# Kernel optimization log

Measured on AMD Instinct MI355X. Metric: run time of the kernel, lower is better.

Reference implementation:

```python
import jax, jax.numpy as jnp
import numpy as np

H = 20  # hidden size (hard-coded in the module)

def setup_inputs() -> dict:
    key = jax.random.key(0)
    ks = jax.random.split(key, 7)
    B, T = 4096, 1000
    s = 1.0 / np.sqrt(H)  # torch default init bound for RNN/Linear
    x = jax.random.normal(ks[0], (B, T, 1), dtype=jnp.float32)
    W_ih = jax.random.uniform(ks[1], (H, 1), jnp.float32, -s, s)
    W_hh = jax.random.uniform(ks[2], (H, H), jnp.float32, -s, s)
    b_ih = jax.random.uniform(ks[3], (H,), jnp.float32, -s, s)
    b_hh = jax.random.uniform(ks[4], (H,), jnp.float32, -s, s)
    fc_w = jax.random.uniform(ks[5], (1, H), jnp.float32, -s, s)
    fc_b = jax.random.uniform(ks[6], (1,), jnp.float32, -s, s)
    return {"x": x, "W_ih": W_ih, "W_hh": W_hh, "b_ih": b_ih,
            "b_hh": b_hh, "fc_w": fc_w, "fc_b": fc_b}

def reference(x, W_ih, W_hh, b_ih, b_hh, fc_w, fc_b):
    # x: [B, T, 1] -> time-major [T, B, 1] for scan
    B = x.shape[0]
    xt = jnp.swapaxes(x, 0, 1)
    # precompute input projection for all timesteps: [T, B, H]
    xproj = jnp.einsum('tbi,hi->tbh', xt, W_ih) + b_ih + b_hh
    h0 = jnp.zeros((B, H), dtype=x.dtype)
    def step(h, xp_t):
        h_new = jax.nn.relu(xp_t + h @ W_hh.T)
        return h_new, None
    h_last, _ = jax.lax.scan(step, h0, xproj)
    # only the last hidden state feeds the head: fc1(rnn_out[:, -1, :])
    out = h_last @ fc_w.T + fc_b  # [B, 1]
    return out
```

## Files before the change

kernel.cpp:

```cpp
#include <hip/hip_runtime.h>


#define TT 1000

typedef float v2f __attribute__((ext_vector_type(2)));

struct Col { v2f p01, p23; float v4; };

#define PIN(v)  asm volatile("" : "+v"(v))
__device__ __forceinline__ void pinc(Col& c) {
    PIN(c.p01); PIN(c.p23); PIN(c.v4);
}
__device__ __forceinline__ void keepc(const Col& c) {
    asm volatile("" :: "v"(c.p01), "v"(c.p23), "v"(c.v4));
}

template <int CTRL>
__device__ __forceinline__ float dpp_f(float v) {
    return __int_as_float(__builtin_amdgcn_update_dpp(
        0, __float_as_int(v), CTRL, 0xF, 0xF, true));
}

#define QP_XOR1 0xB1
#define QP_XOR2 0x4E
#define ROR4   0x124
#define ROR8   0x128

template <int HALF, int C1, int C2>
__device__ __forceinline__ void step(v2f xp, v2f& h01, v2f& h23, float& h4,
                                     const Col& wc0, const Col& wc1,
                                     const Col& wc2, const Col& wc3,
                                     const Col& wc4,
                                     const Col& wih, const Col& bias) {
    const v2f xs = (HALF == 0) ? xp.xx : xp.yy;
    const float xt = (HALF == 0) ? xp.x : xp.y;

    v2f  A01 = __builtin_elementwise_fma(xs, wih.p01, bias.p01);
    v2f  A23 = __builtin_elementwise_fma(xs, wih.p23, bias.p23);
    float a4 = __builtin_fmaf(xt, wih.v4, bias.v4);

#define KCOL(hs, hk, wc)                                           \
    A01 = __builtin_elementwise_fma(hs, (wc).p01, A01);            \
    A23 = __builtin_elementwise_fma(hs, (wc).p23, A23);            \
    a4  = __builtin_fmaf(hk, (wc).v4, a4);
    KCOL(h01.xx, h01.x, wc0)
    KCOL(h01.yy, h01.y, wc1)
    KCOL(h23.xx, h23.x, wc2)
    KCOL(h23.yy, h23.y, wc3)
    { const v2f h4s = {h4, h4};
      KCOL(h4s, h4, wc4) }
#undef KCOL

    float b0 = A01.x, b1 = A01.y, b2 = A23.x, b3 = A23.y, b4 = a4;
    {
        float t0 = dpp_f<C1>(b0), t1 = dpp_f<C1>(b1), t2 = dpp_f<C1>(b2),
              t3 = dpp_f<C1>(b3), t4 = dpp_f<C1>(b4);
        b0 += t0; b1 += t1; b2 += t2; b3 += t3; b4 += t4;
    }
    {
        float t0 = dpp_f<C2>(b0), t1 = dpp_f<C2>(b1), t2 = dpp_f<C2>(b2),
              t3 = dpp_f<C2>(b3), t4 = dpp_f<C2>(b4);
        b0 += t0; b1 += t1; b2 += t2; b3 += t3; b4 += t4;
    }

    const v2f z = {0.f, 0.f};
    v2f r01 = {b0, b1};
    v2f r23 = {b2, b3};
    h01 = __builtin_elementwise_max(r01, z);
    h23 = __builtin_elementwise_max(r23, z);
    h4  = fmaxf(b4, 0.f);
}

__global__ void
__attribute__((amdgpu_flat_work_group_size(64, 64), amdgpu_waves_per_eu(1, 1)))
rnn_os_kernel(const float* __restrict__ x,
              const float* __restrict__ W_ih,
              const float* __restrict__ W_hh,
              const float* __restrict__ b_ih,
              const float* __restrict__ b_hh,
              const float* __restrict__ fc_w,
              const float* __restrict__ fc_b,
              float* __restrict__ out) {
    const int tid = blockIdx.x * 64 + threadIdx.x;
    const int b   = tid >> 4;
    const int gl  = tid & 15;
    const int a   = gl >> 2;
    const int bq  = gl & 3;

    Col we0, we1, we2, we3, we4;
    Col wo0, wo1, wo2, wo3, wo4;
#define LOADC(wk, k, rbase, cbase)                                            \
    { (wk).p01 = (v2f){ W_hh[((rbase) + 0) * 20 + (cbase) + (k)],             \
                        W_hh[((rbase) + 1) * 20 + (cbase) + (k)] };           \
      (wk).p23 = (v2f){ W_hh[((rbase) + 2) * 20 + (cbase) + (k)],             \
                        W_hh[((rbase) + 3) * 20 + (cbase) + (k)] };           \
      (wk).v4  =        W_hh[((rbase) + 4) * 20 + (cbase) + (k)]; }
    LOADC(we0, 0, a * 5, bq * 5) LOADC(we1, 1, a * 5, bq * 5)
    LOADC(we2, 2, a * 5, bq * 5) LOADC(we3, 3, a * 5, bq * 5)
    LOADC(we4, 4, a * 5, bq * 5)
    LOADC(wo0, 0, bq * 5, a * 5) LOADC(wo1, 1, bq * 5, a * 5)
    LOADC(wo2, 2, bq * 5, a * 5) LOADC(wo3, 3, bq * 5, a * 5)
    LOADC(wo4, 4, bq * 5, a * 5)
#undef LOADC

    const bool eact = (bq == 0);
    const bool oact = (a == 0);
    Col wie, bie, wio, bio;
#define LOADIB(wv, bv, base, act)                                             \
    { const float* pw = W_ih + (base);                                        \
      const float* p1 = b_ih + (base);                                        \
      const float* p2 = b_hh + (base);                                        \
      (wv).p01 = (v2f){ (act) ? pw[0] : 0.f, (act) ? pw[1] : 0.f };           \
      (wv).p23 = (v2f){ (act) ? pw[2] : 0.f, (act) ? pw[3] : 0.f };           \
      (wv).v4  =        (act) ? pw[4] : 0.f;                                  \
      (bv).p01 = (v2f){ (act) ? (p1[0] + p2[0]) : 0.f,                        \
                        (act) ? (p1[1] + p2[1]) : 0.f };                      \
      (bv).p23 = (v2f){ (act) ? (p1[2] + p2[2]) : 0.f,                        \
                        (act) ? (p1[3] + p2[3]) : 0.f };                      \
      (bv).v4  =        (act) ? (p1[4] + p2[4]) : 0.f; }
    LOADIB(wie, bie, a * 5,  eact)
    LOADIB(wio, bio, bq * 5, oact)
#undef LOADIB

    pinc(we0); pinc(we1); pinc(we2); pinc(we3); pinc(we4);
    pinc(wo0); pinc(wo1); pinc(wo2); pinc(wo3); pinc(wo4);
    pinc(wie); pinc(bie); pinc(wio); pinc(bio);

    v2f h01 = {0.f, 0.f}, h23 = {0.f, 0.f};
    float h4 = 0.f;

    const float* __restrict__ xb = x + (size_t)b * TT;

#define LOAD10(P, off)                                  \
    P##0 = *(const float4*)(xb + (off));                \
    P##1 = *(const float4*)(xb + (off) + 4);            \
    P##2 = *(const float4*)(xb + (off) + 8);            \
    P##3 = *(const float4*)(xb + (off) + 12);           \
    P##4 = *(const float4*)(xb + (off) + 16);           \
    P##5 = *(const float4*)(xb + (off) + 20);           \
    P##6 = *(const float4*)(xb + (off) + 24);           \
    P##7 = *(const float4*)(xb + (off) + 28);           \
    P##8 = *(const float4*)(xb + (off) + 32);           \
    P##9 = *(const float4*)(xb + (off) + 36);

#define STEP_E(xp, H) step<H, QP_XOR1, QP_XOR2>(xp, h01, h23, h4, we0, we1, we2, we3, we4, wie, bie);
#define STEP_O(xp, H) step<H, ROR4,    ROR8   >(xp, h01, h23, h4, wo0, wo1, wo2, wo3, wo4, wio, bio);
#define RUN4(Q) {                                       \
        const v2f qlo = {Q.x, Q.y};                     \
        const v2f qhi = {Q.z, Q.w};                     \
        STEP_E(qlo, 0) STEP_O(qlo, 1)                   \
        STEP_E(qhi, 0) STEP_O(qhi, 1) }
#define RUN40(P) RUN4(P##0) RUN4(P##1) RUN4(P##2) RUN4(P##3) RUN4(P##4) \
                 RUN4(P##5) RUN4(P##6) RUN4(P##7) RUN4(P##8) RUN4(P##9)

    float4 A0, A1, A2, A3, A4, A5, A6, A7, A8, A9;
    float4 B0, B1, B2, B3, B4, B5, B6, B7, B8, B9;
    LOAD10(A, 0)
    LOAD10(B, 40)

    for (int it = 0; it < 12; ++it) {
        const int base = it * 80;
        const int nb = (it < 11) ? base + 120 : 960;

        RUN40(A)
        LOAD10(A, base + 80)
        RUN40(B)
        LOAD10(B, nb)
    }
    RUN40(A)

#undef RUN40
#undef RUN4
#undef STEP_E
#undef STEP_O
#undef LOAD10

    keepc(we0); keepc(we1); keepc(we2); keepc(we3); keepc(we4);
    keepc(wo0); keepc(wo1); keepc(wo2); keepc(wo3); keepc(wo4);
    keepc(wie); keepc(bie); keepc(wio); keepc(bio);

    float dot;
    {
        const float* pf = fc_w + bq * 5;
        float f0 = oact ? pf[0] : 0.f, f1 = oact ? pf[1] : 0.f;
        float f2 = oact ? pf[2] : 0.f, f3 = oact ? pf[3] : 0.f;
        float f4 = oact ? pf[4] : 0.f;
        dot = h01.x * f0;
        dot = __builtin_fmaf(h01.y, f1, dot);
        dot = __builtin_fmaf(h23.x, f2, dot);
        dot = __builtin_fmaf(h23.y, f3, dot);
        dot = __builtin_fmaf(h4,    f4, dot);
    }
    dot += __shfl_xor(dot, 1, 16);
    dot += __shfl_xor(dot, 2, 16);
    dot += __shfl_xor(dot, 4, 16);
    dot += __shfl_xor(dot, 8, 16);

    if (gl == 0)
        out[b] = dot + fc_b[0];
}

extern "C" void kernel_launch(void* const* d_in, const int* in_sizes, int n_in,
                              void* d_out, int out_size, void* d_ws, size_t ws_size,
                              hipStream_t stream) {
    const float* x    = (const float*)d_in[0];
    const float* W_ih = (const float*)d_in[1];
    const float* W_hh = (const float*)d_in[2];
    const float* b_ih = (const float*)d_in[3];
    const float* b_hh = (const float*)d_in[4];
    const float* fc_w = (const float*)d_in[5];
    const float* fc_b = (const float*)d_in[6];
    float* out = (float*)d_out;

    const int block = 64;
    const int grid  = (4096 * 16) / block;
    rnn_os_kernel<<<grid, block, 0, stream>>>(x, W_ih, W_hh, b_ih, b_hh,
                                              fc_w, fc_b, out);
}
```

Measured before the change: 146.7 us.

## Pack two batch rows per 16-lane group using packed v2f lanes

Each 16-lane group now processes two batch elements at once, with the v2f packed-FMA lanes holding the two batch rows instead of two hidden units. This halves the grid and makes every FMA a full packed operation, but doubles the DPP reductions per lane. The x prefetch shrinks from 20 float4 registers ahead to 4 small float4 loads per two iterations. The aims are better packed-math use and fewer waves, at the cost of more latency exposure on the x loads and fewer waves to hide the serial recurrence.

```diff
diff --git a/kernel.cpp b/kernel.cpp
--- a/kernel.cpp
+++ b/kernel.cpp
@@ -5,14 +5,29 @@
 
 typedef float v2f __attribute__((ext_vector_type(2)));
 
-struct Col { v2f p01, p23; float v4; };
+struct WRole {
+    v2f w01[5], w23[5];
+    v2f w4a, w4b, w4c;
+    v2f wih01, wih23, wih4;
+    v2f b01, b23, b4;
+};
 
 #define PIN(v)  asm volatile("" : "+v"(v))
-__device__ __forceinline__ void pinc(Col& c) {
-    PIN(c.p01); PIN(c.p23); PIN(c.v4);
-}
-__device__ __forceinline__ void keepc(const Col& c) {
-    asm volatile("" :: "v"(c.p01), "v"(c.p23), "v"(c.v4));
+__device__ __forceinline__ void pinw(WRole& W) {
+    PIN(W.w01[0]); PIN(W.w01[1]); PIN(W.w01[2]); PIN(W.w01[3]); PIN(W.w01[4]);
+    PIN(W.w23[0]); PIN(W.w23[1]); PIN(W.w23[2]); PIN(W.w23[3]); PIN(W.w23[4]);
+    PIN(W.w4a); PIN(W.w4b); PIN(W.w4c);
+    PIN(W.wih01); PIN(W.wih23); PIN(W.wih4);
+    PIN(W.b01); PIN(W.b23); PIN(W.b4);
+}
+__device__ __forceinline__ void keepw(const WRole& W) {
+    asm volatile("" :: "v"(W.w01[0]), "v"(W.w01[1]), "v"(W.w01[2]),
+                       "v"(W.w01[3]), "v"(W.w01[4]));
+    asm volatile("" :: "v"(W.w23[0]), "v"(W.w23[1]), "v"(W.w23[2]),
+                       "v"(W.w23[3]), "v"(W.w23[4]));
+    asm volatile("" :: "v"(W.w4a), "v"(W.w4b), "v"(W.w4c));
+    asm volatile("" :: "v"(W.wih01), "v"(W.wih23), "v"(W.wih4),
+                       "v"(W.b01), "v"(W.b23), "v"(W.b4));
 }
 
 template <int CTRL>
@@ -26,49 +41,55 @@
 #define ROR4   0x124
 #define ROR8   0x128
 
-template <int HALF, int C1, int C2>
-__device__ __forceinline__ void step(v2f xp, v2f& h01, v2f& h23, float& h4,
-                                     const Col& wc0, const Col& wc1,
-                                     const Col& wc2, const Col& wc3,
-                                     const Col& wc4,
-                                     const Col& wih, const Col& bias) {
-    const v2f xs = (HALF == 0) ? xp.xx : xp.yy;
-    const float xt = (HALF == 0) ? xp.x : xp.y;
-
-    v2f  A01 = __builtin_elementwise_fma(xs, wih.p01, bias.p01);
-    v2f  A23 = __builtin_elementwise_fma(xs, wih.p23, bias.p23);
-    float a4 = __builtin_fmaf(xt, wih.v4, bias.v4);
-
-#define KCOL(hs, hk, wc)                                           \
-    A01 = __builtin_elementwise_fma(hs, (wc).p01, A01);            \
-    A23 = __builtin_elementwise_fma(hs, (wc).p23, A23);            \
-    a4  = __builtin_fmaf(hk, (wc).v4, a4);
-    KCOL(h01.xx, h01.x, wc0)
-    KCOL(h01.yy, h01.y, wc1)
-    KCOL(h23.xx, h23.x, wc2)
-    KCOL(h23.yy, h23.y, wc3)
-    { const v2f h4s = {h4, h4};
-      KCOL(h4s, h4, wc4) }
-#undef KCOL
-
-    float b0 = A01.x, b1 = A01.y, b2 = A23.x, b3 = A23.y, b4 = a4;
+template <int C1, int C2>
+__device__ __forceinline__ void step(v2f xp, v2f& h0, v2f& h1, v2f& h2,
+                                     v2f& h3, v2f& h4, const WRole& W) {
+    v2f a0 = __builtin_elementwise_fma(xp, W.wih01.xx, W.b01.xx);
+    v2f a1 = __builtin_elementwise_fma(xp, W.wih01.yy, W.b01.yy);
+    v2f a2 = __builtin_elementwise_fma(xp, W.wih23.xx, W.b23.xx);
+    v2f a3 = __builtin_elementwise_fma(xp, W.wih23.yy, W.b23.yy);
+    v2f a4 = __builtin_elementwise_fma(xp, W.wih4.xx,  W.b4.xx);
+
+#define MK(HS, W0, W1, W2, W3, W4)                         \
+    a0 = __builtin_elementwise_fma(HS, W0, a0);            \
+    a1 = __builtin_elementwise_fma(HS, W1, a1);            \
+    a2 = __builtin_elementwise_fma(HS, W2, a2);            \
+    a3 = __builtin_elementwise_fma(HS, W3, a3);            \
+    a4 = __builtin_elementwise_fma(HS, W4, a4);
+    MK(h0, W.w01[0].xx, W.w01[1].xx, W.w01[2].xx, W.w01[3].xx, W.w01[4].xx)
+    MK(h1, W.w01[0].yy, W.w01[1].yy, W.w01[2].yy, W.w01[3].yy, W.w01[4].yy)
+    MK(h2, W.w23[0].xx, W.w23[1].xx, W.w23[2].xx, W.w23[3].xx, W.w23[4].xx)
+    MK(h3, W.w23[0].yy, W.w23[1].yy, W.w23[2].yy, W.w23[3].yy, W.w23[4].yy)
+    MK(h4, W.w4a.xx,    W.w4a.yy,    W.w4b.xx,    W.w4b.yy,    W.w4c.xx)
+#undef MK
+
+    float u0 = a0.x, p0 = a0.y, u1 = a1.x, p1 = a1.y, u2 = a2.x, p2 = a2.y,
+          u3 = a3.x, p3 = a3.y, u4 = a4.x, p4 = a4.y;
     {
-        float t0 = dpp_f<C1>(b0), t1 = dpp_f<C1>(b1), t2 = dpp_f<C1>(b2),
-              t3 = dpp_f<C1>(b3), t4 = dpp_f<C1>(b4);
-        b0 += t0; b1 += t1; b2 += t2; b3 += t3; b4 += t4;
+        float t0 = dpp_f<C1>(u0), s0 = dpp_f<C1>(p0),
+              t1 = dpp_f<C1>(u1), s1 = dpp_f<C1>(p1),
+              t2 = dpp_f<C1>(u2), s2 = dpp_f<C1>(p2),
+              t3 = dpp_f<C1>(u3), s3 = dpp_f<C1>(p3),
+              t4 = dpp_f<C1>(u4), s4 = dpp_f<C1>(p4);
+        u0 += t0; p0 += s0; u1 += t1; p1 += s1; u2 += t2; p2 += s2;
+        u3 += t3; p3 += s3; u4 += t4; p4 += s4;
     }
     {
-        float t0 = dpp_f<C2>(b0), t1 = dpp_f<C2>(b1), t2 = dpp_f<C2>(b2),
-              t3 = dpp_f<C2>(b3), t4 = dpp_f<C2>(b4);
-        b0 += t0; b1 += t1; b2 += t2; b3 += t3; b4 += t4;
+        float t0 = dpp_f<C2>(u0), s0 = dpp_f<C2>(p0),
+              t1 = dpp_f<C2>(u1), s1 = dpp_f<C2>(p1),
+              t2 = dpp_f<C2>(u2), s2 = dpp_f<C2>(p2),
+              t3 = dpp_f<C2>(u3), s3 = dpp_f<C2>(p3),
+              t4 = dpp_f<C2>(u4), s4 = dpp_f<C2>(p4);
+        u0 += t0; p0 += s0; u1 += t1; p1 += s1; u2 += t2; p2 += s2;
+        u3 += t3; p3 += s3; u4 += t4; p4 += s4;
     }
 
     const v2f z = {0.f, 0.f};
-    v2f r01 = {b0, b1};
-    v2f r23 = {b2, b3};
-    h01 = __builtin_elementwise_max(r01, z);
-    h23 = __builtin_elementwise_max(r23, z);
-    h4  = fmaxf(b4, 0.f);
+    h0 = __builtin_elementwise_max((v2f){u0, p0}, z);
+    h1 = __builtin_elementwise_max((v2f){u1, p1}, z);
+    h2 = __builtin_elementwise_max((v2f){u2, p2}, z);
+    h3 = __builtin_elementwise_max((v2f){u3, p3}, z);
+    h4 = __builtin_elementwise_max((v2f){u4, p4}, z);
 }
 
 __global__ void
@@ -82,122 +103,110 @@
               const float* __restrict__ fc_b,
               float* __restrict__ out) {
     const int tid = blockIdx.x * 64 + threadIdx.x;
-    const int b   = tid >> 4;
+    const int pg  = tid >> 4;
     const int gl  = tid & 15;
     const int a   = gl >> 2;
     const int bq  = gl & 3;
 
-    Col we0, we1, we2, we3, we4;
-    Col wo0, wo1, wo2, wo3, wo4;
-#define LOADC(wk, k, rbase, cbase)                                            \
-    { (wk).p01 = (v2f){ W_hh[((rbase) + 0) * 20 + (cbase) + (k)],             \
-                        W_hh[((rbase) + 1) * 20 + (cbase) + (k)] };           \
-      (wk).p23 = (v2f){ W_hh[((rbase) + 2) * 20 + (cbase) + (k)],             \
-                        W_hh[((rbase) + 3) * 20 + (cbase) + (k)] };           \
-      (wk).v4  =        W_hh[((rbase) + 4) * 20 + (cbase) + (k)]; }
-    LOADC(we0, 0, a * 5, bq * 5) LOADC(we1, 1, a * 5, bq * 5)
-    LOADC(we2, 2, a * 5, bq * 5) LOADC(we3, 3, a * 5, bq * 5)
-    LOADC(we4, 4, a * 5, bq * 5)
-    LOADC(wo0, 0, bq * 5, a * 5) LOADC(wo1, 1, bq * 5, a * 5)
-    LOADC(wo2, 2, bq * 5, a * 5) LOADC(wo3, 3, bq * 5, a * 5)
-    LOADC(wo4, 4, bq * 5, a * 5)
-#undef LOADC
-
     const bool eact = (bq == 0);
     const bool oact = (a == 0);
-    Col wie, bie, wio, bio;
-#define LOADIB(wv, bv, base, act)                                             \
-    { const float* pw = W_ih + (base);                                        \
-      const float* p1 = b_ih + (base);                                        \
-      const float* p2 = b_hh + (base);                                        \
-      (wv).p01 = (v2f){ (act) ? pw[0] : 0.f, (act) ? pw[1] : 0.f };           \
-      (wv).p23 = (v2f){ (act) ? pw[2] : 0.f, (act) ? pw[3] : 0.f };           \
-      (wv).v4  =        (act) ? pw[4] : 0.f;                                  \
-      (bv).p01 = (v2f){ (act) ? (p1[0] + p2[0]) : 0.f,                        \
-                        (act) ? (p1[1] + p2[1]) : 0.f };                      \
-      (bv).p23 = (v2f){ (act) ? (p1[2] + p2[2]) : 0.f,                        \
-                        (act) ? (p1[3] + p2[3]) : 0.f };                      \
-      (bv).v4  =        (act) ? (p1[4] + p2[4]) : 0.f; }
-    LOADIB(wie, bie, a * 5,  eact)
-    LOADIB(wio, bio, bq * 5, oact)
-#undef LOADIB
-
-    pinc(we0); pinc(we1); pinc(we2); pinc(we3); pinc(we4);
-    pinc(wo0); pinc(wo1); pinc(wo2); pinc(wo3); pinc(wo4);
-    pinc(wie); pinc(bie); pinc(wio); pinc(bio);
-
-    v2f h01 = {0.f, 0.f}, h23 = {0.f, 0.f};
-    float h4 = 0.f;
-
-    const float* __restrict__ xb = x + (size_t)b * TT;
-
-#define LOAD10(P, off)                                  \
-    P##0 = *(const float4*)(xb + (off));                \
-    P##1 = *(const float4*)(xb + (off) + 4);            \
-    P##2 = *(const float4*)(xb + (off) + 8);            \
-    P##3 = *(const float4*)(xb + (off) + 12);           \
-    P##4 = *(const float4*)(xb + (off) + 16);           \
-    P##5 = *(const float4*)(xb + (off) + 20);           \
-    P##6 = *(const float4*)(xb + (off) + 24);           \
-    P##7 = *(const float4*)(xb + (off) + 28);           \
-    P##8 = *(const float4*)(xb + (off) + 32);           \
-    P##9 = *(const float4*)(xb + (off) + 36);
-
-#define STEP_E(xp, H) step<H, QP_XOR1, QP_XOR2>(xp, h01, h23, h4, we0, we1, we2, we3, we4, wie, bie);
-#define STEP_O(xp, H) step<H, ROR4,    ROR8   >(xp, h01, h23, h4, wo0, wo1, wo2, wo3, wo4, wio, bio);
-#define RUN4(Q) {                                       \
-        const v2f qlo = {Q.x, Q.y};                     \
-        const v2f qhi = {Q.z, Q.w};                     \
-        STEP_E(qlo, 0) STEP_O(qlo, 1)                   \
-        STEP_E(qhi, 0) STEP_O(qhi, 1) }
-#define RUN40(P) RUN4(P##0) RUN4(P##1) RUN4(P##2) RUN4(P##3) RUN4(P##4) \
-                 RUN4(P##5) RUN4(P##6) RUN4(P##7) RUN4(P##8) RUN4(P##9)
-
-    float4 A0, A1, A2, A3, A4, A5, A6, A7, A8, A9;
-    float4 B0, B1, B2, B3, B4, B5, B6, B7, B8, B9;
-    LOAD10(A, 0)
-    LOAD10(B, 40)
-
-    for (int it = 0; it < 12; ++it) {
-        const int base = it * 80;
-        const int nb = (it < 11) ? base + 120 : 960;
-
-        RUN40(A)
-        LOAD10(A, base + 80)
-        RUN40(B)
-        LOAD10(B, nb)
-    }
-    RUN40(A)
-
-#undef RUN40
+
+    WRole We, Wo;
+#define WLOAD(W, RB, CB, ACT)                                                 \
+    { const int rb = (RB), cb = (CB);                                         \
+      for (int r = 0; r < 5; ++r) {                                           \
+          (W).w01[r] = (v2f){ W_hh[(rb + r) * 20 + cb + 0],                   \
+                              W_hh[(rb + r) * 20 + cb + 1] };                 \
+          (W).w23[r] = (v2f){ W_hh[(rb + r) * 20 + cb + 2],                   \
+                              W_hh[(rb + r) * 20 + cb + 3] };                 \
+      }                                                                       \
+      (W).w4a = (v2f){ W_hh[(rb + 0) * 20 + cb + 4],                          \
+                       W_hh[(rb + 1) * 20 + cb + 4] };                        \
+      (W).w4b = (v2f){ W_hh[(rb + 2) * 20 + cb + 4],                          \
+                       W_hh[(rb + 3) * 20 + cb + 4] };                        \
+      (W).w4c = (v2f){ W_hh[(rb + 4) * 20 + cb + 4],                          \
+                       W_hh[(rb + 4) * 20 + cb + 4] };                        \
+      const float* pw = W_ih + rb;                                            \
+      const float* p1 = b_ih + rb;                                            \
+      const float* p2 = b_hh + rb;                                            \
+      (W).wih01 = (v2f){ (ACT) ? pw[0] : 0.f, (ACT) ? pw[1] : 0.f };          \
+      (W).wih23 = (v2f){ (ACT) ? pw[2] : 0.f, (ACT) ? pw[3] : 0.f };          \
+      (W).wih4  = (v2f){ (ACT) ? pw[4] : 0.f, (ACT) ? pw[4] : 0.f };          \
+      (W).b01 = (v2f){ (ACT) ? (p1[0] + p2[0]) : 0.f,                         \
+                       (ACT) ? (p1[1] + p2[1]) : 0.f };                       \
+      (W).b23 = (v2f){ (ACT) ? (p1[2] + p2[2]) : 0.f,                         \
+                       (ACT) ? (p1[3] + p2[3]) : 0.f };                       \
+      (W).b4  = (v2f){ (ACT) ? (p1[4] + p2[4]) : 0.f,                         \
+                       (ACT) ? (p1[4] + p2[4]) : 0.f }; }
+    WLOAD(We, a * 5,  bq * 5, eact)
+    WLOAD(Wo, bq * 5, a * 5,  oact)
+#undef WLOAD
+
+    pinw(We); pinw(Wo);
+
+    v2f h0 = {0.f, 0.f}, h1 = {0.f, 0.f}, h2 = {0.f, 0.f},
+        h3 = {0.f, 0.f}, h4 = {0.f, 0.f};
+
+    const float* __restrict__ xbE = x + (size_t)(2 * pg) * TT;
+    const float* __restrict__ xbO = xbE + TT;
+
+#define STEP_E(XP) step<QP_XOR1, QP_XOR2>(XP, h0, h1, h2, h3, h4, We);
+#define STEP_O(XP) step<ROR4,    ROR8   >(XP, h0, h1, h2, h3, h4, Wo);
+#define RUN4(QE, QO) {                                  \
+        v2f x0 = {QE.x, QO.x}; STEP_E(x0)               \
+        v2f x1 = {QE.y, QO.y}; STEP_O(x1)               \
+        v2f x2 = {QE.z, QO.z}; STEP_E(x2)               \
+        v2f x3 = {QE.w, QO.w}; STEP_O(x3) }
+
+    float4 AE = *(const float4*)(xbE);
+    float4 AO = *(const float4*)(xbO);
+    float4 BE = *(const float4*)(xbE + 4);
+    float4 BO = *(const float4*)(xbO + 4);
+
+    for (int it = 0; it < 124; ++it) {
+        const int p = it * 8;
+        RUN4(AE, AO)
+        AE = *(const float4*)(xbE + p + 8);
+        AO = *(const float4*)(xbO + p + 8);
+        RUN4(BE, BO)
+        BE = *(const float4*)(xbE + p + 12);
+        BO = *(const float4*)(xbO + p + 12);
+    }
+    RUN4(AE, AO)
+    RUN4(BE, BO)
+
 #undef RUN4
 #undef STEP_E
 #undef STEP_O
-#undef LOAD10
-
-    keepc(we0); keepc(we1); keepc(we2); keepc(we3); keepc(we4);
-    keepc(wo0); keepc(wo1); keepc(wo2); keepc(wo3); keepc(wo4);
-    keepc(wie); keepc(bie); keepc(wio); keepc(bio);
-
-    float dot;
+
+    keepw(We); keepw(Wo);
+
+    float dx, dy;
     {
         const float* pf = fc_w + bq * 5;
         float f0 = oact ? pf[0] : 0.f, f1 = oact ? pf[1] : 0.f;
         float f2 = oact ? pf[2] : 0.f, f3 = oact ? pf[3] : 0.f;
         float f4 = oact ? pf[4] : 0.f;
-        dot = h01.x * f0;
-        dot = __builtin_fmaf(h01.y, f1, dot);
-        dot = __builtin_fmaf(h23.x, f2, dot);
-        dot = __builtin_fmaf(h23.y, f3, dot);
-        dot = __builtin_fmaf(h4,    f4, dot);
-    }
-    dot += __shfl_xor(dot, 1, 16);
-    dot += __shfl_xor(dot, 2, 16);
-    dot += __shfl_xor(dot, 4, 16);
-    dot += __shfl_xor(dot, 8, 16);
-
-    if (gl == 0)
-        out[b] = dot + fc_b[0];
+        dx = h0.x * f0;
+        dx = __builtin_fmaf(h1.x, f1, dx);
+        dx = __builtin_fmaf(h2.x, f2, dx);
+        dx = __builtin_fmaf(h3.x, f3, dx);
+        dx = __builtin_fmaf(h4.x, f4, dx);
+        dy = h0.y * f0;
+        dy = __builtin_fmaf(h1.y, f1, dy);
+        dy = __builtin_fmaf(h2.y, f2, dy);
+        dy = __builtin_fmaf(h3.y, f3, dy);
+        dy = __builtin_fmaf(h4.y, f4, dy);
+    }
+    dx += __shfl_xor(dx, 1, 16);  dy += __shfl_xor(dy, 1, 16);
+    dx += __shfl_xor(dx, 2, 16);  dy += __shfl_xor(dy, 2, 16);
+    dx += __shfl_xor(dx, 4, 16);  dy += __shfl_xor(dy, 4, 16);
+    dx += __shfl_xor(dx, 8, 16);  dy += __shfl_xor(dy, 8, 16);
+
+    if (gl == 0) {
+        float2 o = { dx + fc_b[0], dy + fc_b[0] };
+        *(float2*)(out + 2 * pg) = o;
+    }
 }
 
 extern "C" void kernel_launch(void* const* d_in, const int* in_sizes, int n_in,
@@ -213,7 +222,7 @@
     float* out = (float*)d_out;
 
     const int block = 64;
-    const int grid  = (4096 * 16) / block;
+    const int grid  = (2048 * 16) / block;
     rnn_os_kernel<<<grid, block, 0, stream>>>(x, W_ih, W_hh, b_ih, b_hh,
                                               fc_w, fc_b, out);
 }
```

Result: slower. 247.3 us (+68.5%).
